# Optimization experiments

Hardware: AMD Instinct MI355X
Metric: run time of the kernel (lower is better)

Reference implementation:

```python
import jax, jax.numpy as jnp
import numpy as np

E, H, D = 1024, 16, 64
F = 4608          # max_ffn_size = int(1024*3*1.5)
BASE_FFN = 3072   # int(emb*3)
ADAPT = 0.5
CHUNK = 256


def rotate_half(x):
    x1 = x[..., ::2]
    x2 = x[..., 1::2]
    return jnp.stack((-x2, x1), axis=-1).reshape(x.shape[:-1] + (-1,))


def rms_norm(x, w, eps=1e-6):
    x = jnp.where(jnp.isnan(x) | jnp.isinf(x), jnp.zeros_like(x), x)
    rms = jnp.clip(jnp.sqrt(jnp.mean(x * x, axis=-1, keepdims=True) + eps), 1e-6, 1e6)
    return x / rms * w


def setup_inputs() -> dict:
    key = jax.random.key(0)
    ks = jax.random.split(key, 12)
    s = 0.02
    return {
        "x": jax.random.normal(ks[0], (2, 4096, E), dtype=jnp.float32),
        "w_qkv": jax.random.normal(ks[1], (E, 3 * E), dtype=jnp.float32) * s,
        "w_out": jax.random.normal(ks[2], (E, E), dtype=jnp.float32) * s,
        "g1": jnp.ones((E,), dtype=jnp.float32),
        "g2": jnp.ones((E,), dtype=jnp.float32),
        "w_dp1": jax.random.normal(ks[3], (E, E // 4), dtype=jnp.float32) * s,
        "w_dp2": jax.random.normal(ks[4], (E // 4, 1), dtype=jnp.float32) * s,
        "w_gate": jax.random.normal(ks[5], (E, F), dtype=jnp.float32) * s,
        "w_up": jax.random.normal(ks[6], (E, F), dtype=jnp.float32) * s,
        "w_down": jax.random.normal(ks[7], (F, E), dtype=jnp.float32) * s,
        "g_hidden": jnp.ones((F,), dtype=jnp.float32),
    }


def _linear_attention(x, w_qkv, w_out):
    B, L, _ = x.shape
    qkv = (x @ w_qkv).reshape(B, L, 3, H, D).transpose(2, 0, 3, 1, 4)  # [3,B,H,L,D]
    q, k, v = qkv[0], qkv[1], qkv[2]
    # RoPE (start_pos = 0)
    pos = jnp.arange(L, dtype=jnp.float32)
    inv_freq = 1.0 / (10000.0 ** (jnp.arange(0, D, 2, dtype=jnp.float32) / D))
    freqs = pos[:, None] * inv_freq[None, :]
    emb = jnp.concatenate([freqs, freqs], axis=-1)
    cos = jnp.cos(emb)[None, None]
    sin = jnp.sin(emb)[None, None]
    q = q * cos + rotate_half(q) * sin
    k = k * cos + rotate_half(k) * sin
    # elu + 1 feature map
    q = jax.nn.elu(q) + 1.0
    k = jax.nn.elu(k) + 1.0
    # chunk-wise cumulative recurrence (no cache path)
    NC = L // CHUNK
    def to_chunks(t):
        return jnp.moveaxis(t.reshape(B, H, NC, CHUNK, D), 2, 0)  # [NC,B,H,C,D]
    qc, kc, vc = to_chunks(q), to_chunks(k), to_chunks(v)

    def step(carry, inp):
        S, Z = carry  # S:[B,H,D,D], Z:[B,H,D]
        qi, ki, vi = inp
        kv = jnp.einsum('bhld,bhle->bhlde', ki, vi)
        kv_cum = jnp.cumsum(kv, axis=2) + S[:, :, None]
        k_cum = jnp.cumsum(ki, axis=2) + Z[:, :, None]
        num = jnp.einsum('bhld,bhlde->bhle', qi, kv_cum)
        den = jnp.einsum('bhld,bhld->bhl', qi, k_cum)
        return (kv_cum[:, :, -1], k_cum[:, :, -1]), (num, den)

    S0 = jnp.zeros((B, H, D, D), dtype=x.dtype)
    Z0 = jnp.zeros((B, H, D), dtype=x.dtype)
    _, (num, den) = jax.lax.scan(step, (S0, Z0), (qc, kc, vc))
    num = jnp.moveaxis(num, 0, 2).reshape(B, H, L, D)
    den = jnp.moveaxis(den, 0, 2).reshape(B, H, L)
    den = jnp.maximum(den, 1e-6)
    out = num / den[..., None]
    out = out.transpose(0, 2, 1, 3).reshape(B, L, H * D)
    return out @ w_out


def _adaptive_ffn(x, w_dp1, w_dp2, w_gate, w_up, w_down, g_hidden):
    x_mean = x.mean(axis=1)                                   # [B,E]
    dim_ratio = jax.nn.sigmoid(jax.nn.silu(x_mean @ w_dp1) @ w_dp2)  # [B,1]
    ratio = jnp.clip(1.0 + (dim_ratio - 0.5) * 2.0 * ADAPT, 1.0 - ADAPT, 1.0 + ADAPT)
    size = jnp.maximum(1, jnp.floor(BASE_FFN * ratio.mean())).astype(jnp.int32)
    mask = (jnp.arange(F) < size).astype(x.dtype)             # [F]
    gate = jax.nn.silu(x @ w_gate) * mask
    up = (x @ w_up) * mask
    hidden = gate * up
    hidden = jnp.where(jnp.isnan(hidden) | jnp.isinf(hidden), jnp.zeros_like(hidden), hidden)
    # RMSNorm over the first `size` features only (matches sliced torch RMSNorm)
    rms = jnp.sqrt(jnp.sum(hidden * hidden, axis=-1, keepdims=True) / size.astype(x.dtype) + 1e-6)
    rms = jnp.clip(rms, 1e-6, 1e6)
    hidden = hidden / rms * g_hidden * mask                   # padded-to-F hidden
    return hidden @ w_down


def reference(x, w_qkv, w_out, g1, g2, w_dp1, w_dp2, w_gate, w_up, w_down, g_hidden):
    # pre-norm residual block: x + attn(norm1(x)); then x + ffn(norm2(x))
    h = rms_norm(x, g1)
    x = x + _linear_attention(h, w_qkv, w_out)
    h2 = rms_norm(x, g2)
    x = x + _adaptive_ffn(h2, w_dp1, w_dp2, w_gate, w_up, w_down, g_hidden)
    return x
```

## Files before the change

kernel.cpp:

```cpp
#include <hip/hip_runtime.h>
#include <hip/hip_bf16.h>

#define Ee 1024
#define Hh 16
#define Ff 4608
#define Ll 4096
#define Bb 2
#define NCc 16
#define CHk 256

typedef short bf16x8 __attribute__((ext_vector_type(8)));
typedef float f32x4 __attribute__((ext_vector_type(4)));

#define GLD16(g, l) __builtin_amdgcn_global_load_lds( \
    (const __attribute__((address_space(1))) unsigned int*)(g), \
    (__attribute__((address_space(3))) unsigned int*)(l), 16, 0, 0)

__device__ __forceinline__ unsigned short f2bf(float f){
  unsigned int u = __builtin_bit_cast(unsigned int, f);
  u += 0x7fffu + ((u >> 16) & 1u);
  return (unsigned short)(u >> 16);
}
__device__ __forceinline__ float bf2f(unsigned short h){
  unsigned int u = ((unsigned int)h) << 16;
  return __builtin_bit_cast(float, u);
}
__device__ __forceinline__ float fixv(float v){
  return (__builtin_isnan(v) || __builtin_isinf(v)) ? 0.f : v;
}

__global__ __launch_bounds__(256) void wconv_kernel(const float* __restrict__ W,
    unsigned short* __restrict__ WT, int K, int N, const float* __restrict__ scale){
  __shared__ unsigned short T[64][72];
  int k0 = blockIdx.y*64, n0 = blockIdx.x*64;
  int t = threadIdx.x;
  int kr = t>>4, n4 = (t&15)*4;
  #pragma unroll
  for (int it=0; it<4; it++){
    int k = kr + it*16;
    float s = scale ? scale[k0+k] : 1.f;
    float4 v = *(const float4*)(W + (size_t)(k0+k)*N + n0 + n4);
    T[n4+0][k] = f2bf(v.x*s);
    T[n4+1][k] = f2bf(v.y*s);
    T[n4+2][k] = f2bf(v.z*s);
    T[n4+3][k] = f2bf(v.w*s);
  }
  __syncthreads();
  int u = t&7;
  #pragma unroll
  for (int it=0; it<2; it++){
    int n = (t>>3) + it*32;
    *(bf16x8*)(WT + (size_t)(n0+n)*K + k0 + u*8) = *(const bf16x8*)&T[n][u*8];
  }
}

__global__ __launch_bounds__(256) void rmsnorm_kernel(const float* __restrict__ x,
    const float* __restrict__ g, unsigned short* __restrict__ out){
  int row = blockIdx.x; int t = threadIdx.x;
  float4 v = ((const float4*)(x + (size_t)row*Ee))[t];
  v.x=fixv(v.x); v.y=fixv(v.y); v.z=fixv(v.z); v.w=fixv(v.w);
  float ss = v.x*v.x + v.y*v.y + v.z*v.z + v.w*v.w;
  #pragma unroll
  for (int off=32; off>0; off>>=1) ss += __shfl_down(ss, off);
  __shared__ float red[4];
  if ((t&63)==0) red[t>>6] = ss;
  __syncthreads();
  float tot = red[0]+red[1]+red[2]+red[3];
  float rms = sqrtf(tot*(1.f/Ee) + 1e-6f);
  rms = fminf(fmaxf(rms, 1e-6f), 1e6f);
  float inv = 1.f/rms;
  float4 gv = ((const float4*)g)[t];
  uint2 o;
  o.x = (unsigned)f2bf(v.x*inv*gv.x) | ((unsigned)f2bf(v.y*inv*gv.y)<<16);
  o.y = (unsigned)f2bf(v.z*inv*gv.z) | ((unsigned)f2bf(v.w*inv*gv.w)<<16);
  ((uint2*)(out + (size_t)row*Ee))[t] = o;
}

template<int MODE>
__global__ __launch_bounds__(256) void gemm_kernel(
    const unsigned short* __restrict__ A, const unsigned short* __restrict__ Bt,
    void* __restrict__ Cv, int M, int N, int K,
    const float* __restrict__ res, const float* __restrict__ rowscale,
    const float* __restrict__ klim){
  __shared__ __align__(16) unsigned short As[2][4096];
  __shared__ __align__(16) unsigned short Bs[2][4096];
  int tid = threadIdx.x;
  int nbx = gridDim.x;
  int id = blockIdx.y * nbx + blockIdx.x;
  int chunk = (nbx * gridDim.y) >> 3;
  int wg = (id & 7) * chunk + (id >> 3);
  int m0 = (wg / nbx) * 128, n0 = (wg % nbx) * 128;
  int lane = tid & 63, wave = tid >> 6;
  int wm = (wave>>1)*64, wn = (wave&1)*64;
  int lrow = lane & 15;
  int lksw = (((lane>>4) ^ ((lrow>>1)&3)))*8;
  int kend = K;
  if (MODE==2 && klim){
    int sz = (int)klim[0];
    int ke = ((sz + 31) >> 5) << 5;
    kend = ke < K ? ke : K;
  }
  int nk = kend >> 5;
  int s0 = wave*2, s1 = s0+1;
  int r0 = s0*16 + (lane>>2), r1 = s1*16 + (lane>>2);
  int cg = (((lane&3) ^ ((lane>>3)&3))) * 8;
  const unsigned short* a0 = A  + (size_t)(m0+r0)*K + cg;
  const unsigned short* a1 = A  + (size_t)(m0+r1)*K + cg;
  const unsigned short* b0 = Bt + (size_t)(n0+r0)*K + cg;
  const unsigned short* b1 = Bt + (size_t)(n0+r1)*K + cg;
  f32x4 acc[4][4] = {};
  GLD16(a0, &As[0][s0*512]); GLD16(a1, &As[0][s1*512]);
  GLD16(b0, &Bs[0][s0*512]); GLD16(b1, &Bs[0][s1*512]);
  __syncthreads();
  int cur = 0;
  for (int t=0; t<nk; ++t){
    if (t+1 < nk){
      int ko = (t+1) << 5;
      GLD16(a0+ko, &As[cur^1][s0*512]); GLD16(a1+ko, &As[cur^1][s1*512]);
      GLD16(b0+ko, &Bs[cur^1][s0*512]); GLD16(b1+ko, &Bs[cur^1][s1*512]);
    }
    bf16x8 af[4], bfr[4];
    #pragma unroll
    for (int i=0;i<4;i++){
      af[i]  = *(const bf16x8*)&As[cur][(wm + i*16 + lrow)*32 + lksw];
      bfr[i] = *(const bf16x8*)&Bs[cur][(wn + i*16 + lrow)*32 + lksw];
    }
    #pragma unroll
    for (int mi=0;mi<4;mi++)
      #pragma unroll
      for (int ni=0;ni<4;ni++)
        acc[mi][ni] = __builtin_amdgcn_mfma_f32_16x16x32_bf16(af[mi], bfr[ni], acc[mi][ni], 0,0,0);
    __syncthreads();
    cur ^= 1;
  }
  int lg = lane >> 4;
  int rbase = m0 + wm + (lg<<2);
  int cbase = n0 + wn + lrow;
  #pragma unroll
  for (int mi=0;mi<4;mi++){
    #pragma unroll
    for (int r=0;r<4;r++){
      int row = rbase + mi*16 + r;
      float rs = (MODE==2) ? rowscale[row] : 1.f;
      #pragma unroll
      for (int ni=0;ni<4;ni++){
        int col = cbase + ni*16;
        float v = acc[mi][ni][r];
        if (MODE==0){
          ((unsigned short*)Cv)[(size_t)row*N + col] = f2bf(v);
        } else if (MODE==1){
          ((float*)Cv)[(size_t)row*N + col] = v + res[(size_t)row*N + col];
        } else {
          ((float*)Cv)[(size_t)row*N + col] = v*rs + res[(size_t)row*N + col];
        }
      }
    }
  }
}

__global__ __launch_bounds__(256) void gateup_kernel(
    const unsigned short* __restrict__ A, const unsigned short* __restrict__ Gt,
    const unsigned short* __restrict__ Ut, unsigned short* __restrict__ Hid,
    const float* __restrict__ scal){
  __shared__ __align__(16) unsigned short As[2][4096];
  __shared__ __align__(16) unsigned short Bg[2][4096];
  __shared__ __align__(16) unsigned short Bu[2][4096];
  int tid = threadIdx.x;
  int nbx = gridDim.x;
  int id = blockIdx.y * nbx + blockIdx.x;
  int chunk = (nbx * gridDim.y) >> 3;
  int wg = (id & 7) * chunk + (id >> 3);
  int m0 = (wg / nbx) * 128, n0 = (wg % nbx) * 128;
  int size = (int)scal[0];
  if (n0 >= size){
    int r = tid >> 1, cb = n0 + (tid&1)*64;
    unsigned short* hp = Hid + (size_t)(m0+r)*Ff + cb;
    bf16x8 z = {};
    #pragma unroll
    for (int i=0;i<8;i++) *(bf16x8*)(hp + i*8) = z;
    return;
  }
  int lane = tid & 63, wave = tid >> 6;
  int wm = (wave>>1)*64, wn = (wave&1)*64;
  int lrow = lane & 15;
  int lksw = (((lane>>4) ^ ((lrow>>1)&3)))*8;
  int s0 = wave*2, s1 = s0+1;
  int r0 = s0*16 + (lane>>2), r1 = s1*16 + (lane>>2);
  int cg = (((lane&3) ^ ((lane>>3)&3))) * 8;
  const unsigned short* a0 = A  + (size_t)(m0+r0)*Ee + cg;
  const unsigned short* a1 = A  + (size_t)(m0+r1)*Ee + cg;
  const unsigned short* g0 = Gt + (size_t)(n0+r0)*Ee + cg;
  const unsigned short* g1p= Gt + (size_t)(n0+r1)*Ee + cg;
  const unsigned short* u0 = Ut + (size_t)(n0+r0)*Ee + cg;
  const unsigned short* u1 = Ut + (size_t)(n0+r1)*Ee + cg;
  f32x4 ag[4][4] = {}, au[4][4] = {};
  GLD16(a0, &As[0][s0*512]); GLD16(a1, &As[0][s1*512]);
  GLD16(g0, &Bg[0][s0*512]); GLD16(g1p,&Bg[0][s1*512]);
  GLD16(u0, &Bu[0][s0*512]); GLD16(u1, &Bu[0][s1*512]);
  __syncthreads();
  int cur = 0;
  for (int t=0; t<32; ++t){
    if (t+1 < 32){
      int ko = (t+1) << 5;
      GLD16(a0+ko, &As[cur^1][s0*512]); GLD16(a1+ko, &As[cur^1][s1*512]);
      GLD16(g0+ko, &Bg[cur^1][s0*512]); GLD16(g1p+ko,&Bg[cur^1][s1*512]);
      GLD16(u0+ko, &Bu[cur^1][s0*512]); GLD16(u1+ko, &Bu[cur^1][s1*512]);
    }
    bf16x8 af[4], bg4[4], bu4[4];
    #pragma unroll
    for (int i=0;i<4;i++){
      af[i]  = *(const bf16x8*)&As[cur][(wm + i*16 + lrow)*32 + lksw];
      bg4[i] = *(const bf16x8*)&Bg[cur][(wn + i*16 + lrow)*32 + lksw];
      bu4[i] = *(const bf16x8*)&Bu[cur][(wn + i*16 + lrow)*32 + lksw];
    }
    #pragma unroll
    for (int mi=0;mi<4;mi++)
      #pragma unroll
      for (int ni=0;ni<4;ni++){
        ag[mi][ni] = __builtin_amdgcn_mfma_f32_16x16x32_bf16(af[mi], bg4[ni], ag[mi][ni], 0,0,0);
        au[mi][ni] = __builtin_amdgcn_mfma_f32_16x16x32_bf16(af[mi], bu4[ni], au[mi][ni], 0,0,0);
      }
    __syncthreads();
    cur ^= 1;
  }
  int lg = lane >> 4;
  int rbase = m0 + wm + (lg<<2);
  int cbase = n0 + wn + lrow;
  #pragma unroll
  for (int mi=0;mi<4;mi++){
    #pragma unroll
    for (int r=0;r<4;r++){
      int row = rbase + mi*16 + r;
      #pragma unroll
      for (int ni=0;ni<4;ni++){
        int col = cbase + ni*16;
        float g = ag[mi][ni][r], u = au[mi][ni][r];
        float hv = (g * (1.f/(1.f+expf(-g)))) * u;
        if (col >= size) hv = 0.f;
        if (__builtin_isnan(hv) || __builtin_isinf(hv)) hv = 0.f;
        Hid[(size_t)row*Ff + col] = f2bf(hv);
      }
    }
  }
}

__global__ __launch_bounds__(256) void rope_kernel(unsigned short* __restrict__ qkv){
  size_t idx = (size_t)blockIdx.x*256 + threadIdx.x;
  int i = (int)(idx & 31);
  int h = (int)((idx>>5) & 15);
  size_t bl = idx >> 9;
  int pos = (int)(bl & (Ll-1));
  int d0 = 2*i, d1 = d0+1;
  size_t base = bl*3072 + (size_t)h*64 + d0;
  const float LOG1E4_D32 = 0.2878231366242557f;
  float e0 = (float)(d0 < 32 ? d0 : d0-32);
  float e1 = (float)(d1 < 32 ? d1 : d1-32);
  float f0 = pos * expf(-e0*LOG1E4_D32);
  float f1 = pos * expf(-e1*LOG1E4_D32);
  float s0,c0,s1,c1;
  sincosf(f0,&s0,&c0); sincosf(f1,&s1,&c1);
  unsigned int* qp = (unsigned int*)(qkv + base);
  unsigned int qv = *qp;
  float q0 = bf2f((unsigned short)(qv&0xffff)), q1 = bf2f((unsigned short)(qv>>16));
  float r0 = q0*c0 - q1*s0;
  float r1 = q1*c1 + q0*s1;
  r0 = r0>0.f ? r0+1.f : expf(r0);
  r1 = r1>0.f ? r1+1.f : expf(r1);
  *qp = (unsigned)f2bf(r0) | ((unsigned)f2bf(r1)<<16);
  unsigned int* kp = (unsigned int*)(qkv + base + 1024);
  unsigned int kv = *kp;
  float k0v = bf2f((unsigned short)(kv&0xffff)), k1v = bf2f((unsigned short)(kv>>16));
  float t0 = k0v*c0 - k1v*s0;
  float t1 = k1v*c1 + k0v*s1;
  t0 = t0>0.f ? t0+1.f : expf(t0);
  t1 = t1>0.f ? t1+1.f : expf(t1);
  *kp = (unsigned)f2bf(t0) | ((unsigned)f2bf(t1)<<16);
}

__global__ __launch_bounds__(256) void chunksum_kernel(const unsigned short* __restrict__ qkv,
    float* __restrict__ Ssum){
  __shared__ __align__(16) unsigned short Kt[64][72];
  __shared__ __align__(16) unsigned short Vt[80][72];
  int c = blockIdx.x, bh = blockIdx.y;
  int b = bh >> 4, h = bh & 15;
  int tid = threadIdx.x, lane = tid & 63, wave = tid >> 6;
  int lr = lane & 15, lg = lane >> 4;
  f32x4 acc[5] = {};
  {
    int r16 = tid >> 4, m4 = (tid & 15) * 4;
    unsigned short val = (r16 == 0) ? (unsigned short)0x3F80 : (unsigned short)0;
    #pragma unroll
    for (int u=0; u<4; u++) Vt[64 + r16][m4 + u] = val;
  }
  for (int t=0; t<4; ++t){
    __syncthreads();
    #pragma unroll
    for (int i=0; i<2; i++){
      int tau = tid + i*256;
      int m = tau & 63, dg = (tau >> 6) * 8;
      size_t g = ((size_t)(b*Ll + c*CHk + t*64 + m))*3072 + h*64 + dg;
      bf16x8 kv = *(const bf16x8*)(qkv + g + 1024);
      bf16x8 vv = *(const bf16x8*)(qkv + g + 2048);
      #pragma unroll
      for (int u=0; u<8; u++){
        Kt[dg+u][m] = (unsigned short)kv[u];
        Vt[dg+u][m] = (unsigned short)vv[u];
      }
    }
    __syncthreads();
    #pragma unroll
    for (int kk=0; kk<2; kk++){
      bf16x8 af = *(const bf16x8*)&Kt[wave*16 + lr][kk*32 + lg*8];
      #pragma unroll
      for (int ni=0; ni<5; ni++){
        bf16x8 vf = *(const bf16x8*)&Vt[ni*16 + lr][kk*32 + lg*8];
        acc[ni] = __builtin_amdgcn_mfma_f32_16x16x32_bf16(af, vf, acc[ni], 0,0,0);
      }
    }
  }
  float* S = Ssum + ((size_t)bh*NCc + c)*4160;
  int j = wave*16 + lg*4;
  #pragma unroll
  for (int ni=0; ni<4; ni++)
    #pragma unroll
    for (int r=0; r<4; r++)
      S[(size_t)(j+r)*64 + ni*16 + lr] = acc[ni][r];
  if (lr == 0){
    #pragma unroll
    for (int r=0; r<4; r++) S[4096 + j + r] = acc[4][r];
  }
}

__global__ __launch_bounds__(256) void prefix_kernel(const float* __restrict__ Ssum,
    float* __restrict__ Spre){
  int bh = blockIdx.x; int t = threadIdx.x;
  size_t base = (size_t)bh*NCc*4160;
  for (int e=t; e<4160; e+=256){
    float acc = 0.f;
    #pragma unroll
    for (int c=0;c<NCc;c++){
      Spre[base + (size_t)c*4160 + e] = acc;
      acc += Ssum[base + (size_t)c*4160 + e];
    }
  }
}

__global__ __launch_bounds__(256, 2) void attnout_kernel(const unsigned short* __restrict__ qkv,
    const float* __restrict__ Spre, unsigned short* __restrict__ attn){
  __shared__ __align__(16) unsigned short SpT[64][72];
  __shared__ __align__(16) unsigned short Ks[64][72];
  __shared__ __align__(16) unsigned short Vt[64][72];
  __shared__ __align__(16) unsigned short P[4][64][72];
  __shared__ float qZd[256];
  int c = blockIdx.x, bh = blockIdx.y;
  int b = bh >> 4, h = bh & 15;
  int tid = threadIdx.x, lane = tid & 63, wave = tid >> 6;
  int lr = lane & 15, lg = lane >> 4;
  const float* Sp = Spre + ((size_t)bh*NCc + c)*4160;

  {
    float zacc = 0.f;
    const unsigned short* qp = qkv + ((size_t)(b*Ll + c*CHk + tid))*3072 + (size_t)h*64;
    #pragma unroll
    for (int g8=0; g8<8; g8++){
      bf16x8 qv = *(const bf16x8*)(qp + g8*8);
      #pragma unroll
      for (int u=0; u<8; u++) zacc += bf2f((unsigned short)qv[u]) * Sp[4096 + g8*8 + u];
    }
    qZd[tid] = zacc;
  }
  #pragma unroll
  for (int i=0; i<2; i++){
    int tau = tid + i*256;
    int j = tau & 63, dg = (tau >> 6) * 8;
    const float* sp = Sp + j*64 + dg;
    #pragma unroll
    for (int u=0; u<8; u++) SpT[dg+u][j] = f2bf(sp[u]);
  }
  bf16x8 af[4][2];
  #pragma unroll
  for (int mi=0; mi<4; mi++){
    size_t qrow = ((size_t)(b*Ll + c*CHk + wave*64 + mi*16 + lr))*3072 + (size_t)h*64;
    #pragma unroll
    for (int kk=0; kk<2; kk++)
      af[mi][kk] = *(const bf16x8*)(qkv + qrow + kk*32 + lg*8);
  }
  __syncthreads();
  f32x4 accO[4][4] = {};
  #pragma unroll
  for (int kk=0; kk<2; kk++){
    #pragma unroll
    for (int ni=0; ni<4; ni++){
      bf16x8 bsp = *(const bf16x8*)&SpT[ni*16 + lr][kk*32 + lg*8];
      #pragma unroll
      for (int mi=0; mi<4; mi++)
        accO[mi][ni] = __builtin_amdgcn_mfma_f32_16x16x32_bf16(af[mi][kk], bsp, accO[mi][ni], 0,0,0);
    }
  }
  f32x4 den4[4] = {};
  for (int t=0; t<4; ++t){
    __syncthreads();
    #pragma unroll
    for (int i=0; i<2; i++){
      int tau = tid + i*256;
      int m = tau & 63, dg = (tau >> 6) * 8;
      size_t g = ((size_t)(b*Ll + c*CHk + t*64 + m))*3072 + h*64 + dg;
      *(bf16x8*)&Ks[m][dg] = *(const bf16x8*)(qkv + g + 1024);
      bf16x8 vv = *(const bf16x8*)(qkv + g + 2048);
      #pragma unroll
      for (int u=0; u<8; u++) Vt[dg+u][m] = (unsigned short)vv[u];
    }
    __syncthreads();
    if (wave < t) continue;
    f32x4 sacc[4][4] = {};
    #pragma unroll
    for (int kk=0; kk<2; kk++){
      #pragma unroll
      for (int ni=0; ni<4; ni++){
        bf16x8 kf = *(const bf16x8*)&Ks[ni*16 + lr][kk*32 + lg*8];
        #pragma unroll
        for (int mi=0; mi<4; mi++)
          sacc[mi][ni] = __builtin_amdgcn_mfma_f32_16x16x32_bf16(af[mi][kk], kf, sacc[mi][ni], 0,0,0);
      }
    }
    unsigned short (*Pw)[72] = P[wave];
    bool diag = (t == wave);
    #pragma unroll
    for (int mi=0; mi<4; mi++){
      #pragma unroll
      for (int r=0; r<4; r++){
        int q_l = mi*16 + lg*4 + r;
        float rs = 0.f;
        #pragma unroll
        for (int ni=0; ni<4; ni++){
          int m_l = ni*16 + lr;
          float v = sacc[mi][ni][r];
          if (diag && m_l > q_l) v = 0.f;
          rs += v;
          Pw[q_l][m_l] = f2bf(v);
        }
        rs += __shfl_xor(rs, 1);
        rs += __shfl_xor(rs, 2);
        rs += __shfl_xor(rs, 4);
        rs += __shfl_xor(rs, 8);
        den4[mi][r] += rs;
      }
    }
    #pragma unroll
    for (int kk=0; kk<2; kk++){
      bf16x8 pa[4], vf[4];
      #pragma unroll
      for (int mi=0; mi<4; mi++) pa[mi] = *(const bf16x8*)&Pw[mi*16 + lr][kk*32 + lg*8];
      #pragma unroll
      for (int ni=0; ni<4; ni++) vf[ni] = *(const bf16x8*)&Vt[ni*16 + lr][kk*32 + lg*8];
      #pragma unroll
      for (int mi=0; mi<4; mi++)
        #pragma unroll
        for (int ni=0; ni<4; ni++)
          accO[mi][ni] = __builtin_amdgcn_mfma_f32_16x16x32_bf16(pa[mi], vf[ni], accO[mi][ni], 0,0,0);
    }
  }
  #pragma unroll
  for (int mi=0; mi<4; mi++){
    #pragma unroll
    for (int r=0; r<4; r++){
      int q_l = mi*16 + lg*4 + r;
      float dtot = den4[mi][r] + qZd[wave*64 + q_l];
      float inv = 1.f / fmaxf(dtot, 1e-6f);
      size_t l = (size_t)(b*Ll + c*CHk + wave*64 + q_l);
      unsigned short* op = attn + l*Ee + h*64 + lr;
      #pragma unroll
      for (int ni=0; ni<4; ni++)
        op[ni*16] = f2bf(accO[mi][ni][r] * inv);
    }
  }
}

__global__ __launch_bounds__(256) void colmean1_kernel(const unsigned short* __restrict__ h2,
    float* __restrict__ partial){
  int e = blockIdx.x*256 + threadIdx.x;
  int ly = blockIdx.y;
  int b = blockIdx.z;
  int l0 = ly * 128;
  float s = 0.f;
  for (int l=l0; l<l0+128; l++) s += bf2f(h2[((size_t)(b*Ll + l))*Ee + e]);
  partial[((size_t)(b*32 + ly))*Ee + e] = s;
}
__global__ __launch_bounds__(256) void colmean2_kernel(const float* __restrict__ partial,
    float* __restrict__ xmean){
  int e = blockIdx.x*256 + threadIdx.x;
  int b = blockIdx.y;
  float s = 0.f;
  #pragma unroll
  for (int ly=0; ly<32; ly++) s += partial[((size_t)(b*32 + ly))*Ee + e];
  xmean[b*Ee + e] = s * (1.f/Ll);
}

__global__ __launch_bounds__(256) void dimpred_kernel(const float* __restrict__ xmean,
    const float* __restrict__ w_dp1, const float* __restrict__ w_dp2,
    float* __restrict__ scalars){
  __shared__ float red[256];
  __shared__ float ratio_s[2];
  int t = threadIdx.x;
  for (int b=0;b<2;b++){
    float s = 0.f;
    for (int k=0;k<1024;k++) s += xmean[b*Ee + k] * w_dp1[k*256 + t];
    float sil = s * (1.f/(1.f+expf(-s)));
    red[t] = sil * w_dp2[t];
    __syncthreads();
    for (int off=128; off>0; off>>=1){
      if (t<off) red[t] += red[t+off];
      __syncthreads();
    }
    if (t==0){
      float dr = 1.f/(1.f+expf(-red[0]));
      float ratio = 1.f + (dr-0.5f)*1.0f;
      ratio = fminf(fmaxf(ratio, 0.5f), 1.5f);
      ratio_s[b] = ratio;
    }
    __syncthreads();
  }
  if (t==0){
    float rm = 0.5f*(ratio_s[0]+ratio_s[1]);
    float size_f = floorf(3072.f * rm);
    if (size_f < 1.f) size_f = 1.f;
    scalars[0] = size_f;
  }
}

__global__ __launch_bounds__(256) void rowrms_kernel(const unsigned short* __restrict__ Hid,
    const float* __restrict__ scal, float* __restrict__ invr){
  int row = blockIdx.x; int t = threadIdx.x;
  float size_f = scal[0];
  int c8max = ((int)size_f + 7) >> 3;
  float ss = 0.f;
  for (int c8 = t; c8 < c8max; c8 += 256){
    bf16x8 v = *(const bf16x8*)(Hid + (size_t)row*Ff + c8*8);
    #pragma unroll
    for (int u=0;u<8;u++){ float f = bf2f((unsigned short)v[u]); ss += f*f; }
  }
  #pragma unroll
  for (int off=32; off>0; off>>=1) ss += __shfl_down(ss, off);
  __shared__ float red[4];
  if ((t&63)==0) red[t>>6] = ss;
  __syncthreads();
  if (t==0){
    float tot = red[0]+red[1]+red[2]+red[3];
    float rms = sqrtf(tot/size_f + 1e-6f);
    rms = fminf(fmaxf(rms, 1e-6f), 1e6f);
    invr[row] = 1.f/rms;
  }
}

extern "C" void kernel_launch(void* const* d_in, const int* in_sizes, int n_in,
                              void* d_out, int out_size, void* d_ws, size_t ws_size,
                              hipStream_t stream){
  const float* x      = (const float*)d_in[0];
  const float* w_qkv  = (const float*)d_in[1];
  const float* w_out  = (const float*)d_in[2];
  const float* g1     = (const float*)d_in[3];
  const float* g2     = (const float*)d_in[4];
  const float* w_dp1  = (const float*)d_in[5];
  const float* w_dp2  = (const float*)d_in[6];
  const float* w_gate = (const float*)d_in[7];
  const float* w_up   = (const float*)d_in[8];
  const float* w_down = (const float*)d_in[9];
  const float* g_hid  = (const float*)d_in[10];
  float* out = (float*)d_out;

  char* w = (char*)d_ws;
  size_t o = 0;
  auto alloc = [&](size_t bytes)->char*{ char* p = w + o; o += (bytes + 255) & ~255ull; return p; };
  unsigned short* R1   = (unsigned short*)alloc((size_t)8192*1024*2);
  float*          x2   = (float*)alloc((size_t)8192*1024*4);
  char*           R2   = alloc((size_t)8192*4608*2);
  unsigned short* qkvT = (unsigned short*)alloc((size_t)3072*1024*2);
  unsigned short* outT = (unsigned short*)alloc((size_t)1024*1024*2);
  char*           W2   = alloc((size_t)3*4608*1024*2);
  float*       partial = (float*)alloc((size_t)64*1024*4);
  float*         xmean = (float*)alloc(2048*4);
  float*          scal = (float*)alloc(64);
  float*          invr = (float*)alloc(8192*4);

  unsigned short* qkv    = (unsigned short*)R2;
  unsigned short* hidden = (unsigned short*)R2;
  float* Ssum = (float*)W2;
  float* Spre = Ssum + (size_t)512*4160;
  unsigned short* gateT = (unsigned short*)W2;
  unsigned short* upT   = gateT + (size_t)4608*1024;
  unsigned short* downT = upT   + (size_t)4608*1024;

  wconv_kernel<<<dim3(3072/64, 1024/64),256,0,stream>>>(w_qkv, qkvT, 1024, 3072, nullptr);
  wconv_kernel<<<dim3(1024/64, 1024/64),256,0,stream>>>(w_out, outT, 1024, 1024, nullptr);

  rmsnorm_kernel<<<8192,256,0,stream>>>(x, g1, R1);
  gemm_kernel<0><<<dim3(3072/128, 8192/128),256,0,stream>>>(R1, qkvT, qkv,
      8192,3072,1024, nullptr,nullptr,nullptr);
  rope_kernel<<<16384,256,0,stream>>>(qkv);
  chunksum_kernel<<<dim3(NCc,Bb*Hh),256,0,stream>>>(qkv, Ssum);
  prefix_kernel<<<Bb*Hh,256,0,stream>>>(Ssum, Spre);
  attnout_kernel<<<dim3(NCc,Bb*Hh),256,0,stream>>>(qkv, Spre, R1);

  wconv_kernel<<<dim3(4608/64, 1024/64),256,0,stream>>>(w_gate, gateT, 1024, 4608, nullptr);
  wconv_kernel<<<dim3(4608/64, 1024/64),256,0,stream>>>(w_up,   upT,   1024, 4608, nullptr);
  wconv_kernel<<<dim3(1024/64, 4608/64),256,0,stream>>>(w_down, downT, 4608, 1024, g_hid);

  gemm_kernel<1><<<dim3(1024/128, 8192/128),256,0,stream>>>(R1, outT, x2,
      8192,1024,1024, x,nullptr,nullptr);
  rmsnorm_kernel<<<8192,256,0,stream>>>(x2, g2, R1);
  colmean1_kernel<<<dim3(4,32,2),256,0,stream>>>(R1, partial);
  colmean2_kernel<<<dim3(4,2),256,0,stream>>>(partial, xmean);
  dimpred_kernel<<<1,256,0,stream>>>(xmean, w_dp1, w_dp2, scal);
  gateup_kernel<<<dim3(4608/128, 8192/128),256,0,stream>>>(R1, gateT, upT, hidden, scal);
  rowrms_kernel<<<8192,256,0,stream>>>(hidden, scal, invr);
  gemm_kernel<2><<<dim3(1024/128, 8192/128),256,0,stream>>>(hidden, downT, out,
      8192,1024,4608, x2, invr, scal);
}
```

Measured before the change: 563.1 us.

## Enlarge GEMM and gate/up tiles to 256x128 with 512-thread blocks

Doubles the M dimension of each block tile in the generic GEMM and the fused gate/up kernel to 256 rows, using 8 waves per block. The separate A/B shared-memory buffers become one unified buffer, and each wave now issues a fixed number of global-to-LDS loads across the combined A and B tiles. The aim is better reuse of the weight tiles and fewer blocks, which cuts global traffic per FLOP. In exchange, LDS use per block rises (up to 64KB in gate/up) and there are half as many blocks, which may hurt occupancy and load balance. The out-projection and down GEMMs now have only 256 blocks.

```diff
diff --git a/kernel.cpp b/kernel.cpp
--- a/kernel.cpp
+++ b/kernel.cpp
@@ -77,19 +77,18 @@
 }
 
 template<int MODE>
-__global__ __launch_bounds__(256) void gemm_kernel(
+__global__ __launch_bounds__(512) void gemm_kernel(
     const unsigned short* __restrict__ A, const unsigned short* __restrict__ Bt,
     void* __restrict__ Cv, int M, int N, int K,
     const float* __restrict__ res, const float* __restrict__ rowscale,
     const float* __restrict__ klim){
-  __shared__ __align__(16) unsigned short As[2][4096];
-  __shared__ __align__(16) unsigned short Bs[2][4096];
+  __shared__ __align__(16) unsigned short S[2][12288];
   int tid = threadIdx.x;
   int nbx = gridDim.x;
   int id = blockIdx.y * nbx + blockIdx.x;
   int chunk = (nbx * gridDim.y) >> 3;
   int wg = (id & 7) * chunk + (id >> 3);
-  int m0 = (wg / nbx) * 128, n0 = (wg % nbx) * 128;
+  int m0 = (wg / nbx) * 256, n0 = (wg % nbx) * 128;
   int lane = tid & 63, wave = tid >> 6;
   int wm = (wave>>1)*64, wn = (wave&1)*64;
   int lrow = lane & 15;
@@ -101,29 +100,32 @@
     kend = ke < K ? ke : K;
   }
   int nk = kend >> 5;
-  int s0 = wave*2, s1 = s0+1;
-  int r0 = s0*16 + (lane>>2), r1 = s1*16 + (lane>>2);
+  int segr = lane >> 2;
   int cg = (((lane&3) ^ ((lane>>3)&3))) * 8;
-  const unsigned short* a0 = A  + (size_t)(m0+r0)*K + cg;
-  const unsigned short* a1 = A  + (size_t)(m0+r1)*K + cg;
-  const unsigned short* b0 = Bt + (size_t)(n0+r0)*K + cg;
-  const unsigned short* b1 = Bt + (size_t)(n0+r1)*K + cg;
+  const unsigned short* gp[3];
+  int loff[3];
+  #pragma unroll
+  for (int i=0;i<3;i++){
+    int g = wave*3 + i;
+    if (g < 16){ gp[i] = A  + (size_t)(m0 + g*16 + segr)*K + cg;       loff[i] = g*512 + lane*8; }
+    else       { gp[i] = Bt + (size_t)(n0 + (g-16)*16 + segr)*K + cg;  loff[i] = 8192 + (g-16)*512 + lane*8; }
+  }
   f32x4 acc[4][4] = {};
-  GLD16(a0, &As[0][s0*512]); GLD16(a1, &As[0][s1*512]);
-  GLD16(b0, &Bs[0][s0*512]); GLD16(b1, &Bs[0][s1*512]);
+  #pragma unroll
+  for (int i=0;i<3;i++) GLD16(gp[i], &S[0][loff[i] - lane*8]);
   __syncthreads();
   int cur = 0;
   for (int t=0; t<nk; ++t){
     if (t+1 < nk){
       int ko = (t+1) << 5;
-      GLD16(a0+ko, &As[cur^1][s0*512]); GLD16(a1+ko, &As[cur^1][s1*512]);
-      GLD16(b0+ko, &Bs[cur^1][s0*512]); GLD16(b1+ko, &Bs[cur^1][s1*512]);
+      #pragma unroll
+      for (int i=0;i<3;i++) GLD16(gp[i]+ko, &S[cur^1][loff[i] - lane*8]);
     }
     bf16x8 af[4], bfr[4];
     #pragma unroll
     for (int i=0;i<4;i++){
-      af[i]  = *(const bf16x8*)&As[cur][(wm + i*16 + lrow)*32 + lksw];
-      bfr[i] = *(const bf16x8*)&Bs[cur][(wn + i*16 + lrow)*32 + lksw];
+      af[i]  = *(const bf16x8*)&S[cur][(wm + i*16 + lrow)*32 + lksw];
+      bfr[i] = *(const bf16x8*)&S[cur][8192 + (wn + i*16 + lrow)*32 + lksw];
     }
     #pragma unroll
     for (int mi=0;mi<4;mi++)
@@ -158,19 +160,17 @@
   }
 }
 
-__global__ __launch_bounds__(256) void gateup_kernel(
+__global__ __launch_bounds__(512) void gateup_kernel(
     const unsigned short* __restrict__ A, const unsigned short* __restrict__ Gt,
     const unsigned short* __restrict__ Ut, unsigned short* __restrict__ Hid,
     const float* __restrict__ scal){
-  __shared__ __align__(16) unsigned short As[2][4096];
-  __shared__ __align__(16) unsigned short Bg[2][4096];
-  __shared__ __align__(16) unsigned short Bu[2][4096];
+  __shared__ __align__(16) unsigned short S[2][16384];
   int tid = threadIdx.x;
   int nbx = gridDim.x;
   int id = blockIdx.y * nbx + blockIdx.x;
   int chunk = (nbx * gridDim.y) >> 3;
   int wg = (id & 7) * chunk + (id >> 3);
-  int m0 = (wg / nbx) * 128, n0 = (wg % nbx) * 128;
+  int m0 = (wg / nbx) * 256, n0 = (wg % nbx) * 128;
   int size = (int)scal[0];
   if (n0 >= size){
     int r = tid >> 1, cb = n0 + (tid&1)*64;
@@ -184,34 +184,34 @@
   int wm = (wave>>1)*64, wn = (wave&1)*64;
   int lrow = lane & 15;
   int lksw = (((lane>>4) ^ ((lrow>>1)&3)))*8;
-  int s0 = wave*2, s1 = s0+1;
-  int r0 = s0*16 + (lane>>2), r1 = s1*16 + (lane>>2);
+  int segr = lane >> 2;
   int cg = (((lane&3) ^ ((lane>>3)&3))) * 8;
-  const unsigned short* a0 = A  + (size_t)(m0+r0)*Ee + cg;
-  const unsigned short* a1 = A  + (size_t)(m0+r1)*Ee + cg;
-  const unsigned short* g0 = Gt + (size_t)(n0+r0)*Ee + cg;
-  const unsigned short* g1p= Gt + (size_t)(n0+r1)*Ee + cg;
-  const unsigned short* u0 = Ut + (size_t)(n0+r0)*Ee + cg;
-  const unsigned short* u1 = Ut + (size_t)(n0+r1)*Ee + cg;
+  const unsigned short* gp[4];
+  int loff[4];
+  #pragma unroll
+  for (int i=0;i<4;i++){
+    int g = wave*4 + i;
+    if (g < 16)      { gp[i] = A  + (size_t)(m0 + g*16 + segr)*Ee + cg;       loff[i] = g*512; }
+    else if (g < 24) { gp[i] = Gt + (size_t)(n0 + (g-16)*16 + segr)*Ee + cg;  loff[i] = 8192 + (g-16)*512; }
+    else             { gp[i] = Ut + (size_t)(n0 + (g-24)*16 + segr)*Ee + cg;  loff[i] = 12288 + (g-24)*512; }
+  }
   f32x4 ag[4][4] = {}, au[4][4] = {};
-  GLD16(a0, &As[0][s0*512]); GLD16(a1, &As[0][s1*512]);
-  GLD16(g0, &Bg[0][s0*512]); GLD16(g1p,&Bg[0][s1*512]);
-  GLD16(u0, &Bu[0][s0*512]); GLD16(u1, &Bu[0][s1*512]);
+  #pragma unroll
+  for (int i=0;i<4;i++) GLD16(gp[i], &S[0][loff[i]]);
   __syncthreads();
   int cur = 0;
   for (int t=0; t<32; ++t){
     if (t+1 < 32){
       int ko = (t+1) << 5;
-      GLD16(a0+ko, &As[cur^1][s0*512]); GLD16(a1+ko, &As[cur^1][s1*512]);
-      GLD16(g0+ko, &Bg[cur^1][s0*512]); GLD16(g1p+ko,&Bg[cur^1][s1*512]);
-      GLD16(u0+ko, &Bu[cur^1][s0*512]); GLD16(u1+ko, &Bu[cur^1][s1*512]);
+      #pragma unroll
+      for (int i=0;i<4;i++) GLD16(gp[i]+ko, &S[cur^1][loff[i]]);
     }
     bf16x8 af[4], bg4[4], bu4[4];
     #pragma unroll
     for (int i=0;i<4;i++){
-      af[i]  = *(const bf16x8*)&As[cur][(wm + i*16 + lrow)*32 + lksw];
-      bg4[i] = *(const bf16x8*)&Bg[cur][(wn + i*16 + lrow)*32 + lksw];
-      bu4[i] = *(const bf16x8*)&Bu[cur][(wn + i*16 + lrow)*32 + lksw];
+      af[i]  = *(const bf16x8*)&S[cur][(wm + i*16 + lrow)*32 + lksw];
+      bg4[i] = *(const bf16x8*)&S[cur][8192  + (wn + i*16 + lrow)*32 + lksw];
+      bu4[i] = *(const bf16x8*)&S[cur][12288 + (wn + i*16 + lrow)*32 + lksw];
     }
     #pragma unroll
     for (int mi=0;mi<4;mi++)
@@ -594,7 +594,7 @@
   wconv_kernel<<<dim3(1024/64, 1024/64),256,0,stream>>>(w_out, outT, 1024, 1024, nullptr);
 
   rmsnorm_kernel<<<8192,256,0,stream>>>(x, g1, R1);
-  gemm_kernel<0><<<dim3(3072/128, 8192/128),256,0,stream>>>(R1, qkvT, qkv,
+  gemm_kernel<0><<<dim3(3072/128, 8192/256),512,0,stream>>>(R1, qkvT, qkv,
       8192,3072,1024, nullptr,nullptr,nullptr);
   rope_kernel<<<16384,256,0,stream>>>(qkv);
   chunksum_kernel<<<dim3(NCc,Bb*Hh),256,0,stream>>>(qkv, Ssum);
@@ -605,14 +605,14 @@
   wconv_kernel<<<dim3(4608/64, 1024/64),256,0,stream>>>(w_up,   upT,   1024, 4608, nullptr);
   wconv_kernel<<<dim3(1024/64, 4608/64),256,0,stream>>>(w_down, downT, 4608, 1024, g_hid);
 
-  gemm_kernel<1><<<dim3(1024/128, 8192/128),256,0,stream>>>(R1, outT, x2,
+  gemm_kernel<1><<<dim3(1024/128, 8192/256),512,0,stream>>>(R1, outT, x2,
       8192,1024,1024, x,nullptr,nullptr);
   rmsnorm_kernel<<<8192,256,0,stream>>>(x2, g2, R1);
   colmean1_kernel<<<dim3(4,32,2),256,0,stream>>>(R1, partial);
   colmean2_kernel<<<dim3(4,2),256,0,stream>>>(partial, xmean);
   dimpred_kernel<<<1,256,0,stream>>>(xmean, w_dp1, w_dp2, scal);
-  gateup_kernel<<<dim3(4608/128, 8192/128),256,0,stream>>>(R1, gateT, upT, hidden, scal);
+  gateup_kernel<<<dim3(4608/128, 8192/256),512,0,stream>>>(R1, gateT, upT, hidden, scal);
   rowrms_kernel<<<8192,256,0,stream>>>(hidden, scal, invr);
-  gemm_kernel<2><<<dim3(1024/128, 8192/128),256,0,stream>>>(hidden, downT, out,
+  gemm_kernel<2><<<dim3(1024/128, 8192/256),512,0,stream>>>(hidden, downT, out,
       8192,1024,4608, x2, invr, scal);
 }
```

Result: faster. 514.9 us (-8.6%).
